# Optimization experiments

Measured on AMD Instinct MI355X. Metric: run time of the kernel, lower is better.

## Reference

```python
import jax, jax.numpy as jnp
import numpy as np

B, S, H = 16, 1024, 4
QD, KD, VD = 128, 256, 256


def setup_inputs() -> dict:
    key = jax.random.key(0)
    ks = jax.random.split(key, 12)
    s = 0.02
    return {
        "query": jax.random.normal(ks[0], (B, S, QD), jnp.float32),
        "key": jax.random.normal(ks[1], (B, S, KD), jnp.float32),
        "value": jax.random.normal(ks[2], (B, S, VD), jnp.float32),
        "Wq": jax.random.normal(ks[3], (QD, KD * H), jnp.float32) * s,
        "bq": jnp.zeros((KD * H,), jnp.float32),
        "Wk": jax.random.normal(ks[4], (KD, KD * H), jnp.float32) * s,
        "bk": jnp.zeros((KD * H,), jnp.float32),
        "Wv": jax.random.normal(ks[5], (VD, VD * H), jnp.float32) * s,
        "bv": jnp.zeros((VD * H,), jnp.float32),
        "Wo": jax.random.normal(ks[6], (VD * H, 8 * VD), jnp.float32) * s,
        "bo": jnp.zeros((8 * VD,), jnp.float32),
        "W1": jax.random.normal(ks[7], (8 * VD, 128), jnp.float32) * s,
        "b1": jnp.zeros((128,), jnp.float32),
        "random_len": S,
    }


def reference(query, key, value, Wq, bq, Wk, bk, Wv, bv, Wo, bo, W1, b1, random_len):
    b = query.shape[0]
    # flat view [B, S, H*D] -> [B, H, S, D], exactly matching torch .view semantics
    tq = (query @ Wq + bq).reshape(b, H, -1, KD)
    tk = (key @ Wk + bk).reshape(b, H, -1, KD)
    tv = (value @ Wv + bv).reshape(b, H, -1, VD)
    # NOTE: original has NO 1/sqrt(d) scaling
    scores = jnp.einsum("bhqd,bhkd->bhqk", tq, tk)  # [B,H,S,S]
    attn = jax.nn.softmax(scores, axis=-1)
    attended = jnp.einsum("bhqk,bhkd->bhqd", attn, tv)  # [B,H,S,VD]
    attended = attended.reshape(b, -1, VD * H)  # [B,S,H*VD]
    out = attended @ Wo + bo  # [B,S,2048]
    out = out.mean(axis=1)  # [B,2048]
    out = out @ W1 + b1  # [B,128]
    return out, attn
```

## Files before the change

### kernel.cpp

```cpp
#include <hip/hip_runtime.h>
#include <hip/hip_bf16.h>

typedef _Float16 half_t;
typedef _Float16 half8 __attribute__((ext_vector_type(8)));
typedef _Float16 half4v __attribute__((ext_vector_type(4)));
typedef float floatx4 __attribute__((ext_vector_type(4)));

__device__ inline void gload16(const half_t* g, half_t* l) {
  __builtin_amdgcn_global_load_lds(
      (const __attribute__((address_space(1))) void*)g,
      (__attribute__((address_space(3))) void*)l, 16, 0, 0);
}

__global__ __launch_bounds__(256) void wtrans_kernel(const float* __restrict__ W,
                                                     half_t* __restrict__ Wt, int K, int N) {
  __shared__ float sm[32][33];
  int n0 = blockIdx.x * 32, k0 = blockIdx.y * 32;
  int x = threadIdx.x & 31, y0 = threadIdx.x >> 5;
#pragma unroll
  for (int yy = 0; yy < 4; ++yy) {
    int y = y0 + yy * 8;
    sm[y][x] = W[(size_t)(k0 + y) * N + n0 + x];
  }
  __syncthreads();
#pragma unroll
  for (int yy = 0; yy < 4; ++yy) {
    int y = y0 + yy * 8;
    Wt[(size_t)(n0 + y) * K + k0 + x] = (half_t)sm[x][y];
  }
}

__global__ __launch_bounds__(256) void wtrans3_kernel(
    const float* __restrict__ Wq, half_t* __restrict__ Wqt,
    const float* __restrict__ Wk, half_t* __restrict__ Wkt,
    const float* __restrict__ Wv, half_t* __restrict__ Wvt) {
  __shared__ float sm[32][33];
  int y = blockIdx.y;
  const float* W; half_t* Wt; int K, k0;
  if (y < 4)       { W = Wq; Wt = Wqt; K = 128; k0 = y * 32; }
  else if (y < 12) { W = Wk; Wt = Wkt; K = 256; k0 = (y - 4) * 32; }
  else             { W = Wv; Wt = Wvt; K = 256; k0 = (y - 12) * 32; }
  int n0 = blockIdx.x * 32;
  int x = threadIdx.x & 31, y0 = threadIdx.x >> 5;
#pragma unroll
  for (int yy = 0; yy < 4; ++yy) {
    int r = y0 + yy * 8;
    sm[r][x] = W[(size_t)(k0 + r) * 1024 + n0 + x];
  }
  __syncthreads();
#pragma unroll
  for (int yy = 0; yy < 4; ++yy) {
    int r = y0 + yy * 8;
    Wt[(size_t)(n0 + r) * K + k0 + x] = (half_t)sm[x][r];
  }
}

template <bool AF32, bool BIAS>
__global__ __launch_bounds__(256) void gemm_nt(
    const float* __restrict__ Af, const half_t* __restrict__ Ah,
    const half_t* __restrict__ Bt, const float* __restrict__ bias,
    half_t* __restrict__ C, int K, int ldc,
    size_t aStrideZ, size_t bStrideZ, size_t cStrideZ) {
  __shared__ half_t sA[128 * 32];
  __shared__ half_t sB[128 * 32];
  const int t = threadIdx.x;
  const int m0 = blockIdx.x * 128;
  const int n0 = blockIdx.y * 128;
  const int z = blockIdx.z;
  const half_t* Bz = Bt + bStrideZ * (size_t)z;
  const int w = t >> 6, lane = t & 63;
  const int wm = w & 1, wn = w >> 1;
  const int lr = lane & 15, lk = lane >> 4;
  const int srow = t >> 2, sg = t & 3;

  floatx4 acc[4][4] = {};

  for (int k0 = 0; k0 < K; k0 += 32) {
    __syncthreads();
#pragma unroll
    for (int rep = 0; rep < 2; ++rep) {
      int row = srow + rep * 64;
      int goff = (sg ^ ((row >> 1) & 3)) * 8;
      half8 hv;
      if constexpr (AF32) {
        const float* p = Af + (size_t)(m0 + row) * K + k0 + sg * 8;
        float4 f0 = *(const float4*)p;
        float4 f1 = *(const float4*)(p + 4);
        hv[0] = (half_t)f0.x; hv[1] = (half_t)f0.y;
        hv[2] = (half_t)f0.z; hv[3] = (half_t)f0.w;
        hv[4] = (half_t)f1.x; hv[5] = (half_t)f1.y;
        hv[6] = (half_t)f1.z; hv[7] = (half_t)f1.w;
      } else {
        const half_t* p = Ah + aStrideZ * (size_t)z + (size_t)(m0 + row) * K + k0 + sg * 8;
        hv = *(const half8*)p;
      }
      *(half8*)&sA[row * 32 + goff] = hv;
      const half_t* q = Bz + (size_t)(n0 + row) * K + k0 + sg * 8;
      *(half8*)&sB[row * 32 + goff] = *(const half8*)q;
    }
    __syncthreads();
    half8 af[4], bf[4];
#pragma unroll
    for (int mt = 0; mt < 4; ++mt) {
      int row = wm * 64 + mt * 16 + lr;
      af[mt] = *(const half8*)&sA[row * 32 + ((lk ^ ((row >> 1) & 3)) * 8)];
    }
#pragma unroll
    for (int nt = 0; nt < 4; ++nt) {
      int row = wn * 64 + nt * 16 + lr;
      bf[nt] = *(const half8*)&sB[row * 32 + ((lk ^ ((row >> 1) & 3)) * 8)];
    }
#pragma unroll
    for (int mt = 0; mt < 4; ++mt)
#pragma unroll
      for (int nt = 0; nt < 4; ++nt)
        acc[mt][nt] = __builtin_amdgcn_mfma_f32_16x16x32_f16(bf[nt], af[mt], acc[mt][nt], 0, 0, 0);
  }

  half_t* Cz = C + cStrideZ * (size_t)z;
#pragma unroll
  for (int mt = 0; mt < 4; ++mt) {
    int m = m0 + wm * 64 + mt * 16 + lr;
#pragma unroll
    for (int nt = 0; nt < 4; ++nt) {
      int nb = n0 + wn * 64 + nt * 16 + lk * 4;
      floatx4 a = acc[mt][nt];
      half4v h;
      if constexpr (BIAS) {
        float4 bv = *(const float4*)&bias[nb];
        h[0] = (half_t)(a[0] + bv.x); h[1] = (half_t)(a[1] + bv.y);
        h[2] = (half_t)(a[2] + bv.z); h[3] = (half_t)(a[3] + bv.w);
      } else {
        h[0] = (half_t)a[0]; h[1] = (half_t)a[1];
        h[2] = (half_t)a[2]; h[3] = (half_t)a[3];
      }
      *(half4v*)&Cz[(size_t)m * ldc + nb] = h;
    }
  }
}

__global__ __launch_bounds__(256) void proj_gemm(
    const float* __restrict__ query, const float* __restrict__ key, const float* __restrict__ value,
    const half_t* __restrict__ Wqt, const half_t* __restrict__ Wkt, const half_t* __restrict__ Wvt,
    const float* __restrict__ bq, const float* __restrict__ bk, const float* __restrict__ bv,
    half_t* __restrict__ Tq, half_t* __restrict__ Tk, half_t* __restrict__ Tv) {
  const int z = blockIdx.z;
  const float* Af = z == 0 ? query : (z == 1 ? key : value);
  const half_t* Bt = z == 0 ? Wqt : (z == 1 ? Wkt : Wvt);
  const float* bias = z == 0 ? bq : (z == 1 ? bk : bv);
  half_t* C = z == 0 ? Tq : (z == 1 ? Tk : Tv);
  const int K = z == 0 ? 128 : 256;

  __shared__ half_t sA[128 * 32];
  __shared__ half_t sB[128 * 32];
  const int t = threadIdx.x;
  const int m0 = blockIdx.x * 128;
  const int n0 = blockIdx.y * 128;
  const int w = t >> 6, lane = t & 63;
  const int wm = w & 1, wn = w >> 1;
  const int lr = lane & 15, lk = lane >> 4;
  const int srow = t >> 2, sg = t & 3;

  floatx4 acc[4][4] = {};

  for (int k0 = 0; k0 < K; k0 += 32) {
    __syncthreads();
#pragma unroll
    for (int rep = 0; rep < 2; ++rep) {
      int row = srow + rep * 64;
      int goff = (sg ^ ((row >> 1) & 3)) * 8;
      const float* p = Af + (size_t)(m0 + row) * K + k0 + sg * 8;
      float4 f0 = *(const float4*)p;
      float4 f1 = *(const float4*)(p + 4);
      half8 hv;
      hv[0] = (half_t)f0.x; hv[1] = (half_t)f0.y;
      hv[2] = (half_t)f0.z; hv[3] = (half_t)f0.w;
      hv[4] = (half_t)f1.x; hv[5] = (half_t)f1.y;
      hv[6] = (half_t)f1.z; hv[7] = (half_t)f1.w;
      *(half8*)&sA[row * 32 + goff] = hv;
      const half_t* q = Bt + (size_t)(n0 + row) * K + k0 + sg * 8;
      *(half8*)&sB[row * 32 + goff] = *(const half8*)q;
    }
    __syncthreads();
    half8 af[4], bf[4];
#pragma unroll
    for (int mt = 0; mt < 4; ++mt) {
      int row = wm * 64 + mt * 16 + lr;
      af[mt] = *(const half8*)&sA[row * 32 + ((lk ^ ((row >> 1) & 3)) * 8)];
    }
#pragma unroll
    for (int nt = 0; nt < 4; ++nt) {
      int row = wn * 64 + nt * 16 + lr;
      bf[nt] = *(const half8*)&sB[row * 32 + ((lk ^ ((row >> 1) & 3)) * 8)];
    }
#pragma unroll
    for (int mt = 0; mt < 4; ++mt)
#pragma unroll
      for (int nt = 0; nt < 4; ++nt)
        acc[mt][nt] = __builtin_amdgcn_mfma_f32_16x16x32_f16(bf[nt], af[mt], acc[mt][nt], 0, 0, 0);
  }

#pragma unroll
  for (int mt = 0; mt < 4; ++mt) {
    int m = m0 + wm * 64 + mt * 16 + lr;
#pragma unroll
    for (int nt = 0; nt < 4; ++nt) {
      int nb = n0 + wn * 64 + nt * 16 + lk * 4;
      floatx4 a = acc[mt][nt];
      float4 bvv = *(const float4*)&bias[nb];
      half4v h;
      h[0] = (half_t)(a[0] + bvv.x); h[1] = (half_t)(a[1] + bvv.y);
      h[2] = (half_t)(a[2] + bvv.z); h[3] = (half_t)(a[3] + bvv.w);
      *(half4v*)&C[(size_t)m * 1024 + nb] = h;
    }
  }
}

__global__ __launch_bounds__(256, 2) void fused_attn_kernel(
    const half_t* __restrict__ Tq, const half_t* __restrict__ Tk,
    float* __restrict__ attn, float* __restrict__ cs) {
  const int z = blockIdx.y;
  const int q0 = blockIdx.x * 32;
  const int t = threadIdx.x;
  const int w = t >> 6, lane = t & 63;
  const int lr = lane & 15, lk = lane >> 4;

  __shared__ half_t sQ[32 * 256];
  __shared__ half_t sK[3][256 * 32];
  __shared__ float sRS[4][32];

  const half_t* Tqz = Tq + (size_t)z * 262144 + (size_t)q0 * 256;
  const half_t* Tkz = Tk + (size_t)z * 262144;

#pragma unroll
  for (int r = 0; r < 4; ++r) {
    int i = r * 256 + w * 64 + lane;
    int row = i >> 5, j8 = i & 31;
    gload16(Tqz + (size_t)row * 256 + ((j8 ^ (row & 7)) * 8), &sQ[(r * 256 + w * 64) * 8]);
  }
#pragma unroll
  for (int sp = 0; sp < 2; ++sp) {
#pragma unroll
    for (int r = 0; r < 4; ++r) {
      int i = r * 256 + w * 64 + lane;
      int sl = i >> 2, kg = i & 3;
      int grow = ((sl >> 6) << 8) + (sl & 63);
      gload16(Tkz + (size_t)grow * 256 + sp * 32 + ((kg ^ ((sl >> 1) & 3)) * 8),
              &sK[sp][(r * 256 + w * 64) * 8]);
    }
  }

  floatx4 acc[2][16] = {};
#pragma unroll
  for (int s = 0; s < 32; ++s) {
    if (s < 31) {
      asm volatile("s_waitcnt vmcnt(4)" ::: "memory");
    } else {
      asm volatile("s_waitcnt vmcnt(0)" ::: "memory");
    }
    __builtin_amdgcn_sched_barrier(0);
    __builtin_amdgcn_s_barrier();

    if (s + 2 < 32) {
      const int sp = s + 2, g2 = sp >> 3, ks2 = sp & 7;
      half_t* base = &sK[sp % 3][0];
#pragma unroll
      for (int r = 0; r < 4; ++r) {
        int i = r * 256 + w * 64 + lane;
        int sl = i >> 2, kg = i & 3;
        int grow = ((sl >> 6) << 8) + g2 * 64 + (sl & 63);
        gload16(Tkz + (size_t)grow * 256 + ks2 * 32 + ((kg ^ ((sl >> 1) & 3)) * 8),
                base + (r * 256 + w * 64) * 8);
      }
    }

    const int g = s >> 3, ks = s & 7;
    const half_t* kb = &sK[s % 3][0];
    const int j8 = ((ks * 4 + lk) ^ (lr & 7)) * 8;
    half8 af0 = *(const half8*)&sQ[lr * 256 + j8];
    half8 af1 = *(const half8*)&sQ[(16 + lr) * 256 + j8];
#pragma unroll
    for (int l = 0; l < 4; ++l) {
      int sl = w * 64 + l * 16 + lr;
      half8 bf = *(const half8*)&kb[sl * 32 + ((lk ^ ((sl >> 1) & 3)) * 8)];
      acc[0][g * 4 + l] = __builtin_amdgcn_mfma_f32_16x16x32_f16(bf, af0, acc[0][g * 4 + l], 0, 0, 0);
      acc[1][g * 4 + l] = __builtin_amdgcn_mfma_f32_16x16x32_f16(bf, af1, acc[1][g * 4 + l], 0, 0, 0);
    }
  }

  float rs0 = 0.0f, rs1 = 0.0f;
#pragma unroll
  for (int nt = 0; nt < 16; ++nt) {
#pragma unroll
    for (int j = 0; j < 4; ++j) {
      float v0 = __expf(acc[0][nt][j]);
      float v1 = __expf(acc[1][nt][j]);
      acc[0][nt][j] = v0; acc[1][nt][j] = v1;
      rs0 += v0; rs1 += v1;
    }
  }
  rs0 += __shfl_xor(rs0, 16); rs0 += __shfl_xor(rs0, 32);
  rs1 += __shfl_xor(rs1, 16); rs1 += __shfl_xor(rs1, 32);
  if (lane < 16) { sRS[w][lane] = rs0; sRS[w][16 + lane] = rs1; }
  __syncthreads();
  float inv0 = 1.0f / (sRS[0][lr] + sRS[1][lr] + sRS[2][lr] + sRS[3][lr]);
  float inv1 = 1.0f / (sRS[0][16 + lr] + sRS[1][16 + lr] + sRS[2][16 + lr] + sRS[3][16 + lr]);

  const int nb = w * 256;
  float* attnz = attn + (size_t)z * 1048576;
  float* csz = cs + (size_t)z * 4096;
#pragma unroll
  for (int nt = 0; nt < 16; ++nt) {
    int n = nb + nt * 16 + lk * 4;
    floatx4 o0, o1;
    o0[0] = acc[0][nt][0] * inv0; o0[1] = acc[0][nt][1] * inv0;
    o0[2] = acc[0][nt][2] * inv0; o0[3] = acc[0][nt][3] * inv0;
    o1[0] = acc[1][nt][0] * inv1; o1[1] = acc[1][nt][1] * inv1;
    o1[2] = acc[1][nt][2] * inv1; o1[3] = acc[1][nt][3] * inv1;
    __builtin_nontemporal_store(o0, (floatx4*)&attnz[(size_t)(q0 + lr) * 1024 + n]);
    __builtin_nontemporal_store(o1, (floatx4*)&attnz[(size_t)(q0 + 16 + lr) * 1024 + n]);
    float c0 = o0[0] + o1[0], c1 = o0[1] + o1[1], c2 = o0[2] + o1[2], c3 = o0[3] + o1[3];
    c0 += __shfl_xor(c0, 4); c0 += __shfl_xor(c0, 8);
    c1 += __shfl_xor(c1, 4); c1 += __shfl_xor(c1, 8);
    c2 += __shfl_xor(c2, 4); c2 += __shfl_xor(c2, 8);
    c3 += __shfl_xor(c3, 4); c3 += __shfl_xor(c3, 8);
    if (lr < 4) {
      float* p = csz + (size_t)lr * 1024 + n;
      atomicAdd(p + 0, c0);
      atomicAdd(p + 1, c1);
      atomicAdd(p + 2, c2);
      atomicAdd(p + 3, c3);
    }
  }
}

__global__ __launch_bounds__(256) void abar_kernel(const float* __restrict__ cs,
                                                   const half_t* __restrict__ Tv,
                                                   float* __restrict__ abar) {
  int b = blockIdx.x, r = blockIdx.y, kc = blockIdx.z;
  int d = threadIdx.x;
  __shared__ float scs[4][128];
  for (int idx = d; idx < 512; idx += 256) {
    int h = idx >> 7, k = idx & 127;
    scs[h][k] = cs[(size_t)(b * 4 + h) * 4096 + (size_t)r * 1024 + kc * 128 + k];
  }
  __syncthreads();
  float acc = 0.0f;
  for (int h = 0; h < 4; ++h) {
    const half_t* tv = Tv + (size_t)(b * 4 + h) * 262144 + (size_t)kc * 32768 + d;
#pragma unroll 4
    for (int k = 0; k < 128; ++k)
      acc += scs[h][k] * (float)tv[(size_t)k * 256];
  }
  atomicAdd(&abar[b * 1024 + r * 256 + d], acc * (1.0f / 1024.0f));
}

__global__ __launch_bounds__(256) void bcomb_kernel(const float* __restrict__ bo,
                                                    const float* __restrict__ W1,
                                                    const float* __restrict__ b1,
                                                    float* __restrict__ bcomb) {
  int t = threadIdx.x;
  int j = t & 127, h = t >> 7;
  float acc = 0.0f;
  for (int k = h * 1024; k < h * 1024 + 1024; ++k)
    acc += bo[k] * W1[(size_t)k * 128 + j];
  __shared__ float sm[2][128];
  sm[h][j] = acc;
  __syncthreads();
  if (t < 128) bcomb[t] = sm[0][t] + sm[1][t] + b1[t];
}

__global__ __launch_bounds__(256) void final2_kernel(const float* __restrict__ abar,
                                                     const half_t* __restrict__ Wcomb,
                                                     const float* __restrict__ bcomb,
                                                     float* __restrict__ out) {
  int b = blockIdx.x, t = threadIdx.x;
  int j = t & 127, h = t >> 7;
  __shared__ float sa[1024];
  __shared__ float sm[2][128];
  for (int i = t; i < 1024; i += 256) sa[i] = abar[(size_t)b * 1024 + i];
  __syncthreads();
  float acc = 0.0f;
  for (int c = h * 512; c < h * 512 + 512; ++c)
    acc += sa[c] * (float)Wcomb[(size_t)c * 128 + j];
  sm[h][j] = acc;
  __syncthreads();
  if (t < 128) out[(size_t)b * 128 + t] = sm[0][t] + sm[1][t] + bcomb[t];
}

extern "C" void kernel_launch(void* const* d_in, const int* in_sizes, int n_in,
                              void* d_out, int out_size, void* d_ws, size_t ws_size,
                              hipStream_t stream) {
  const float* query = (const float*)d_in[0];
  const float* key   = (const float*)d_in[1];
  const float* value = (const float*)d_in[2];
  const float* Wq = (const float*)d_in[3];
  const float* bq = (const float*)d_in[4];
  const float* Wk = (const float*)d_in[5];
  const float* bk = (const float*)d_in[6];
  const float* Wv = (const float*)d_in[7];
  const float* bv = (const float*)d_in[8];
  const float* Wo = (const float*)d_in[9];
  const float* bo = (const float*)d_in[10];
  const float* W1 = (const float*)d_in[11];
  const float* b1 = (const float*)d_in[12];

  char* ws = (char*)d_ws;
  half_t* Tq   = (half_t*)(ws + 0);
  half_t* Tk   = (half_t*)(ws + 33554432);
  half_t* Tv   = (half_t*)(ws + 67108864);
  float*  cs   = (float*)(ws + 100663296);
  float*  abar = (float*)(ws + 101711872);
  half_t* Wqt  = (half_t*)(ws + 101777408);
  half_t* Wkt  = (half_t*)(ws + 102039552);
  half_t* Wvt  = (half_t*)(ws + 102563840);
  half_t* W1t   = (half_t*)(ws + 0);
  half_t* Wcomb = (half_t*)(ws + 524288);
  float*  bcomb = (float*)(ws + 786432);

  float* out  = (float*)d_out;
  float* attn = out + 2048;

  hipMemsetAsync(cs, 0, 1048576 + 65536, stream);

  wtrans3_kernel<<<dim3(32, 20), 256, 0, stream>>>(Wq, Wqt, Wk, Wkt, Wv, Wvt);

  proj_gemm<<<dim3(128, 8, 3), 256, 0, stream>>>(query, key, value, Wqt, Wkt, Wvt,
                                                 bq, bk, bv, Tq, Tk, Tv);

  fused_attn_kernel<<<dim3(32, 64), 256, 0, stream>>>(Tq, Tk, attn, cs);

  wtrans_kernel<<<dim3(4, 64), 256, 0, stream>>>(W1, W1t, 2048, 128);
  gemm_nt<true, false><<<dim3(8, 1, 1), 256, 0, stream>>>(Wo, nullptr, W1t, nullptr, Wcomb, 2048, 128, 0, 0, 0);
  bcomb_kernel<<<1, 256, 0, stream>>>(bo, W1, b1, bcomb);

  abar_kernel<<<dim3(16, 4, 8), 256, 0, stream>>>(cs, Tv, abar);
  final2_kernel<<<16, 256, 0, stream>>>(abar, Wcomb, bcomb, out);
}
```

Before: 651.6 us.

## Merge small prologue/epilogue kernels and remap attention blocks for XCD locality

```diff
diff --git a/kernel.cpp b/kernel.cpp
--- a/kernel.cpp
+++ b/kernel.cpp
@@ -12,130 +12,38 @@
       (__attribute__((address_space(3))) void*)l, 16, 0, 0);
 }
 
-__global__ __launch_bounds__(256) void wtrans_kernel(const float* __restrict__ W,
-                                                     half_t* __restrict__ Wt, int K, int N) {
-  __shared__ float sm[32][33];
-  int n0 = blockIdx.x * 32, k0 = blockIdx.y * 32;
-  int x = threadIdx.x & 31, y0 = threadIdx.x >> 5;
-#pragma unroll
-  for (int yy = 0; yy < 4; ++yy) {
-    int y = y0 + yy * 8;
-    sm[y][x] = W[(size_t)(k0 + y) * N + n0 + x];
-  }
-  __syncthreads();
-#pragma unroll
-  for (int yy = 0; yy < 4; ++yy) {
-    int y = y0 + yy * 8;
-    Wt[(size_t)(n0 + y) * K + k0 + x] = (half_t)sm[x][y];
-  }
-}
-
-__global__ __launch_bounds__(256) void wtrans3_kernel(
+__global__ __launch_bounds__(256) void wtrans4_kernel(
     const float* __restrict__ Wq, half_t* __restrict__ Wqt,
     const float* __restrict__ Wk, half_t* __restrict__ Wkt,
-    const float* __restrict__ Wv, half_t* __restrict__ Wvt) {
+    const float* __restrict__ Wv, half_t* __restrict__ Wvt,
+    const float* __restrict__ W1, half_t* __restrict__ W1t,
+    float* __restrict__ zbase ) {
+  {
+    unsigned gid = (blockIdx.y * 32 + blockIdx.x) * 256 + threadIdx.x;
+    for (unsigned idx = gid; idx < 278528u; idx += 229376u) zbase[idx] = 0.0f;
+  }
   __shared__ float sm[32][33];
   int y = blockIdx.y;
-  const float* W; half_t* Wt; int K, k0;
-  if (y < 4)       { W = Wq; Wt = Wqt; K = 128; k0 = y * 32; }
-  else if (y < 12) { W = Wk; Wt = Wkt; K = 256; k0 = (y - 4) * 32; }
-  else             { W = Wv; Wt = Wvt; K = 256; k0 = (y - 12) * 32; }
-  int n0 = blockIdx.x * 32;
+  const float* W; half_t* Wt; int K, N, k0, n0;
+  if (y < 4)       { W = Wq; Wt = Wqt; K = 128;  N = 1024; k0 = y * 32;        n0 = blockIdx.x * 32; }
+  else if (y < 12) { W = Wk; Wt = Wkt; K = 256;  N = 1024; k0 = (y - 4) * 32;  n0 = blockIdx.x * 32; }
+  else if (y < 20) { W = Wv; Wt = Wvt; K = 256;  N = 1024; k0 = (y - 12) * 32; n0 = blockIdx.x * 32; }
+  else {
+    int idx = (y - 20) * 32 + blockIdx.x;
+    W = W1; Wt = W1t; K = 2048; N = 128;
+    n0 = (idx & 3) * 32; k0 = (idx >> 2) * 32;
+  }
   int x = threadIdx.x & 31, y0 = threadIdx.x >> 5;
 #pragma unroll
   for (int yy = 0; yy < 4; ++yy) {
     int r = y0 + yy * 8;
-    sm[r][x] = W[(size_t)(k0 + r) * 1024 + n0 + x];
+    sm[r][x] = W[(size_t)(k0 + r) * N + n0 + x];
   }
   __syncthreads();
 #pragma unroll
   for (int yy = 0; yy < 4; ++yy) {
     int r = y0 + yy * 8;
     Wt[(size_t)(n0 + r) * K + k0 + x] = (half_t)sm[x][r];
-  }
-}
-
-template <bool AF32, bool BIAS>
-__global__ __launch_bounds__(256) void gemm_nt(
-    const float* __restrict__ Af, const half_t* __restrict__ Ah,
-    const half_t* __restrict__ Bt, const float* __restrict__ bias,
-    half_t* __restrict__ C, int K, int ldc,
-    size_t aStrideZ, size_t bStrideZ, size_t cStrideZ) {
-  __shared__ half_t sA[128 * 32];
-  __shared__ half_t sB[128 * 32];
-  const int t = threadIdx.x;
-  const int m0 = blockIdx.x * 128;
-  const int n0 = blockIdx.y * 128;
-  const int z = blockIdx.z;
-  const half_t* Bz = Bt + bStrideZ * (size_t)z;
-  const int w = t >> 6, lane = t & 63;
-  const int wm = w & 1, wn = w >> 1;
-  const int lr = lane & 15, lk = lane >> 4;
-  const int srow = t >> 2, sg = t & 3;
-
-  floatx4 acc[4][4] = {};
-
-  for (int k0 = 0; k0 < K; k0 += 32) {
-    __syncthreads();
-#pragma unroll
-    for (int rep = 0; rep < 2; ++rep) {
-      int row = srow + rep * 64;
-      int goff = (sg ^ ((row >> 1) & 3)) * 8;
-      half8 hv;
-      if constexpr (AF32) {
-        const float* p = Af + (size_t)(m0 + row) * K + k0 + sg * 8;
-        float4 f0 = *(const float4*)p;
-        float4 f1 = *(const float4*)(p + 4);
-        hv[0] = (half_t)f0.x; hv[1] = (half_t)f0.y;
-        hv[2] = (half_t)f0.z; hv[3] = (half_t)f0.w;
-        hv[4] = (half_t)f1.x; hv[5] = (half_t)f1.y;
-        hv[6] = (half_t)f1.z; hv[7] = (half_t)f1.w;
-      } else {
-        const half_t* p = Ah + aStrideZ * (size_t)z + (size_t)(m0 + row) * K + k0 + sg * 8;
-        hv = *(const half8*)p;
-      }
-      *(half8*)&sA[row * 32 + goff] = hv;
-      const half_t* q = Bz + (size_t)(n0 + row) * K + k0 + sg * 8;
-      *(half8*)&sB[row * 32 + goff] = *(const half8*)q;
-    }
-    __syncthreads();
-    half8 af[4], bf[4];
-#pragma unroll
-    for (int mt = 0; mt < 4; ++mt) {
-      int row = wm * 64 + mt * 16 + lr;
-      af[mt] = *(const half8*)&sA[row * 32 + ((lk ^ ((row >> 1) & 3)) * 8)];
-    }
-#pragma unroll
-    for (int nt = 0; nt < 4; ++nt) {
-      int row = wn * 64 + nt * 16 + lr;
-      bf[nt] = *(const half8*)&sB[row * 32 + ((lk ^ ((row >> 1) & 3)) * 8)];
-    }
-#pragma unroll
-    for (int mt = 0; mt < 4; ++mt)
-#pragma unroll
-      for (int nt = 0; nt < 4; ++nt)
-        acc[mt][nt] = __builtin_amdgcn_mfma_f32_16x16x32_f16(bf[nt], af[mt], acc[mt][nt], 0, 0, 0);
-  }
-
-  half_t* Cz = C + cStrideZ * (size_t)z;
-#pragma unroll
-  for (int mt = 0; mt < 4; ++mt) {
-    int m = m0 + wm * 64 + mt * 16 + lr;
-#pragma unroll
-    for (int nt = 0; nt < 4; ++nt) {
-      int nb = n0 + wn * 64 + nt * 16 + lk * 4;
-      floatx4 a = acc[mt][nt];
-      half4v h;
-      if constexpr (BIAS) {
-        float4 bv = *(const float4*)&bias[nb];
-        h[0] = (half_t)(a[0] + bv.x); h[1] = (half_t)(a[1] + bv.y);
-        h[2] = (half_t)(a[2] + bv.z); h[3] = (half_t)(a[3] + bv.w);
-      } else {
-        h[0] = (half_t)a[0]; h[1] = (half_t)a[1];
-        h[2] = (half_t)a[2]; h[3] = (half_t)a[3];
-      }
-      *(half4v*)&Cz[(size_t)m * ldc + nb] = h;
-    }
   }
 }
 
@@ -219,8 +127,11 @@
 __global__ __launch_bounds__(256, 2) void fused_attn_kernel(
     const half_t* __restrict__ Tq, const half_t* __restrict__ Tk,
     float* __restrict__ attn, float* __restrict__ cs) {
-  const int z = blockIdx.y;
-  const int q0 = blockIdx.x * 32;
+  const int wgid = blockIdx.y * 32 + blockIdx.x;
+  const int xcd = wgid & 7;
+  const int i6 = wgid >> 3;
+  const int z = xcd * 8 + (i6 >> 5);
+  const int q0 = (i6 & 31) * 32;
   const int t = threadIdx.x;
   const int w = t >> 6, lane = t & 63;
   const int lr = lane & 15, lk = lane >> 4;
@@ -334,6 +245,85 @@
   }
 }
 
+__global__ __launch_bounds__(256) void tail_kernel(
+    const float* __restrict__ Wo, const half_t* __restrict__ W1t,
+    const float* __restrict__ W1, const float* __restrict__ bo,
+    const float* __restrict__ b1, half_t* __restrict__ Wcomb,
+    float* __restrict__ bcomb) {
+  const int t = threadIdx.x;
+  if (blockIdx.x == 8) {
+    int j = t & 127, h = t >> 7;
+    float acc = 0.0f;
+    for (int k = h * 1024; k < h * 1024 + 1024; ++k)
+      acc += bo[k] * W1[(size_t)k * 128 + j];
+    __shared__ float sm[2][128];
+    sm[h][j] = acc;
+    __syncthreads();
+    if (t < 128) bcomb[t] = sm[0][t] + sm[1][t] + b1[t];
+    return;
+  }
+  __shared__ half_t sA[128 * 32];
+  __shared__ half_t sB[128 * 32];
+  const int m0 = blockIdx.x * 128;
+  const int w = t >> 6, lane = t & 63;
+  const int wm = w & 1, wn = w >> 1;
+  const int lr = lane & 15, lk = lane >> 4;
+  const int srow = t >> 2, sg = t & 3;
+
+  floatx4 acc[4][4] = {};
+
+  for (int k0 = 0; k0 < 2048; k0 += 32) {
+    __syncthreads();
+#pragma unroll
+    for (int rep = 0; rep < 2; ++rep) {
+      int row = srow + rep * 64;
+      int goff = (sg ^ ((row >> 1) & 3)) * 8;
+      const float* p = Wo + (size_t)(m0 + row) * 2048 + k0 + sg * 8;
+      float4 f0 = *(const float4*)p;
+      float4 f1 = *(const float4*)(p + 4);
+      half8 hv;
+      hv[0] = (half_t)f0.x; hv[1] = (half_t)f0.y;
+      hv[2] = (half_t)f0.z; hv[3] = (half_t)f0.w;
+      hv[4] = (half_t)f1.x; hv[5] = (half_t)f1.y;
+      hv[6] = (half_t)f1.z; hv[7] = (half_t)f1.w;
+      *(half8*)&sA[row * 32 + goff] = hv;
+      const half_t* q = W1t + (size_t)row * 2048 + k0 + sg * 8;
+      *(half8*)&sB[row * 32 + goff] = *(const half8*)q;
+    }
+    __syncthreads();
+    half8 af[4], bf[4];
+#pragma unroll
+    for (int mt = 0; mt < 4; ++mt) {
+      int row = wm * 64 + mt * 16 + lr;
+      af[mt] = *(const half8*)&sA[row * 32 + ((lk ^ ((row >> 1) & 3)) * 8)];
+    }
+#pragma unroll
+    for (int nt = 0; nt < 4; ++nt) {
+      int row = wn * 64 + nt * 16 + lr;
+      bf[nt] = *(const half8*)&sB[row * 32 + ((lk ^ ((row >> 1) & 3)) * 8)];
+    }
+#pragma unroll
+    for (int mt = 0; mt < 4; ++mt)
+#pragma unroll
+      for (int nt = 0; nt < 4; ++nt)
+        acc[mt][nt] = __builtin_amdgcn_mfma_f32_16x16x32_f16(bf[nt], af[mt], acc[mt][nt], 0, 0, 0);
+  }
+
+#pragma unroll
+  for (int mt = 0; mt < 4; ++mt) {
+    int m = m0 + wm * 64 + mt * 16 + lr;
+#pragma unroll
+    for (int nt = 0; nt < 4; ++nt) {
+      int nb = wn * 64 + nt * 16 + lk * 4;
+      floatx4 a = acc[mt][nt];
+      half4v h;
+      h[0] = (half_t)a[0]; h[1] = (half_t)a[1];
+      h[2] = (half_t)a[2]; h[3] = (half_t)a[3];
+      *(half4v*)&Wcomb[(size_t)m * 128 + nb] = h;
+    }
+  }
+}
+
 __global__ __launch_bounds__(256) void abar_kernel(const float* __restrict__ cs,
                                                    const half_t* __restrict__ Tv,
                                                    float* __restrict__ abar) {
@@ -353,21 +343,6 @@
       acc += scs[h][k] * (float)tv[(size_t)k * 256];
   }
   atomicAdd(&abar[b * 1024 + r * 256 + d], acc * (1.0f / 1024.0f));
-}
-
-__global__ __launch_bounds__(256) void bcomb_kernel(const float* __restrict__ bo,
-                                                    const float* __restrict__ W1,
-                                                    const float* __restrict__ b1,
-                                                    float* __restrict__ bcomb) {
-  int t = threadIdx.x;
-  int j = t & 127, h = t >> 7;
-  float acc = 0.0f;
-  for (int k = h * 1024; k < h * 1024 + 1024; ++k)
-    acc += bo[k] * W1[(size_t)k * 128 + j];
-  __shared__ float sm[2][128];
-  sm[h][j] = acc;
-  __syncthreads();
-  if (t < 128) bcomb[t] = sm[0][t] + sm[1][t] + b1[t];
 }
 
 __global__ __launch_bounds__(256) void final2_kernel(const float* __restrict__ abar,
@@ -414,25 +389,21 @@
   half_t* Wqt  = (half_t*)(ws + 101777408);
   half_t* Wkt  = (half_t*)(ws + 102039552);
   half_t* Wvt  = (half_t*)(ws + 102563840);
-  half_t* W1t   = (half_t*)(ws + 0);
-  half_t* Wcomb = (half_t*)(ws + 524288);
-  float*  bcomb = (float*)(ws + 786432);
+  half_t* W1t  = (half_t*)(ws + 103088128);
+  half_t* Wcomb = (half_t*)(ws + 103612416);
+  float*  bcomb = (float*)(ws + 103874560);
 
   float* out  = (float*)d_out;
   float* attn = out + 2048;
 
-  hipMemsetAsync(cs, 0, 1048576 + 65536, stream);
-
-  wtrans3_kernel<<<dim3(32, 20), 256, 0, stream>>>(Wq, Wqt, Wk, Wkt, Wv, Wvt);
+  wtrans4_kernel<<<dim3(32, 28), 256, 0, stream>>>(Wq, Wqt, Wk, Wkt, Wv, Wvt, W1, W1t, cs);
 
   proj_gemm<<<dim3(128, 8, 3), 256, 0, stream>>>(query, key, value, Wqt, Wkt, Wvt,
                                                  bq, bk, bv, Tq, Tk, Tv);
 
   fused_attn_kernel<<<dim3(32, 64), 256, 0, stream>>>(Tq, Tk, attn, cs);
 
-  wtrans_kernel<<<dim3(4, 64), 256, 0, stream>>>(W1, W1t, 2048, 128);
-  gemm_nt<true, false><<<dim3(8, 1, 1), 256, 0, stream>>>(Wo, nullptr, W1t, nullptr, Wcomb, 2048, 128, 0, 0, 0);
-  bcomb_kernel<<<1, 256, 0, stream>>>(bo, W1, b1, bcomb);
+  tail_kernel<<<9, 256, 0, stream>>>(Wo, W1t, W1, bo, b1, Wcomb, bcomb);
 
   abar_kernel<<<dim3(16, 4, 8), 256, 0, stream>>>(cs, Tv, abar);
   final2_kernel<<<16, 256, 0, stream>>>(abar, Wcomb, bcomb, out);
```

New measurement: 694.0 us. 1.07x slower.
